# Optimization experiments

Measured on AMD Instinct MI355X. Metric: run time of the kernel, lower is better.

## Reference

```python
import jax, jax.numpy as jnp
import numpy as np
from math import sqrt

N = 8192      # points
I = 16        # in_channels
H = 64        # hidden_units
O = 64        # out_channels
CUTS = 8      # conv MLP intermediate width
RADIUS = 9.0
GROUPS = 4    # GroupNorm groups
BLK = 128     # i-block size for tiled pairwise reduction (KeOps-style)


def _leaky(x):
    return jnp.where(x >= 0, x, 0.2 * x)


def _group_norm(f, w, b, eps=1e-5):
    # torch GroupNorm applied to (1, C, N): stats per group over (C//G channels x N points)
    n, c = f.shape
    g = f.reshape(n, GROUPS, c // GROUPS)
    m = g.mean(axis=(0, 2), keepdims=True)
    v = ((g - m) ** 2).mean(axis=(0, 2), keepdims=True)
    g = (g - m) * jax.lax.rsqrt(v + eps)
    return g.reshape(n, c) * w + b


def setup_inputs() -> dict:
    key = jax.random.key(0)
    ks = jax.random.split(key, 20)
    U = lambda k, s, lim: jax.random.uniform(k, s, minval=-lim, maxval=lim)
    points = jax.random.normal(ks[0], (N, 3), dtype=jnp.float32)
    nuv = jax.random.normal(ks[1], (N, 3, 3), dtype=jnp.float32)
    features = jax.random.normal(ks[2], (N, I), dtype=jnp.float32)
    # net_in (torch Linear default init)
    W_in1 = U(ks[3], (H, I), 1 / np.sqrt(I)); b_in1 = U(ks[4], (H,), 1 / np.sqrt(I))
    W_in2 = U(ks[5], (H, H), 1 / np.sqrt(H)); b_in2 = U(ks[6], (H,), 1 / np.sqrt(H))
    # conv MLP with custom init from the module
    A1 = jax.random.normal(ks[7], (CUTS, 3), dtype=jnp.float32)
    B1 = jax.random.uniform(ks[8], (CUTS,)) * 0.8 * jnp.sqrt((A1 ** 2).sum(-1))
    A2 = U(ks[9], (H, CUTS), 1 / np.sqrt(CUTS))
    B2 = jax.random.normal(ks[10], (H,)) * 0.5 * jnp.sqrt((A2 ** 2).sum(-1))
    # net_out
    W_out1 = U(ks[11], (O, H), 1 / np.sqrt(H)); b_out1 = U(ks[12], (O,), 1 / np.sqrt(H))
    W_out2 = U(ks[13], (O, O), 1 / np.sqrt(O)); b_out2 = U(ks[14], (O,), 1 / np.sqrt(O))
    return {
        "points": points, "nuv": nuv, "features": features,
        "W_in1": W_in1, "b_in1": b_in1, "W_in2": W_in2, "b_in2": b_in2,
        "gn_in_w": jnp.ones((H,), jnp.float32), "gn_in_b": jnp.zeros((H,), jnp.float32),
        "A1": A1, "B1": B1, "A2": A2, "B2": B2,
        "W_out1": W_out1, "b_out1": b_out1, "W_out2": W_out2, "b_out2": b_out2,
        "gn_out_w": jnp.ones((O,), jnp.float32), "gn_out_b": jnp.zeros((O,), jnp.float32),
    }


def _forward(points, nuv, features, W_in1, b_in1, W_in2, b_in2, gn_in_w, gn_in_b,
             A1, B1, A2, B2, W_out1, b_out1, W_out2, b_out2, gn_out_w, gn_out_b):
    # 1. net_in + GroupNorm
    f = _leaky(features @ W_in1.T + b_in1)
    f = _leaky(f @ W_in2.T + b_in2)
    f = _group_norm(f, gn_in_w, gn_in_b)          # (N, H)
    # 2. quasi-geodesic interaction, tiled over i-blocks (KeOps-style)
    pts = points / (sqrt(2.0) * RADIUS)
    normals = jax.lax.stop_gradient(nuv[:, 0, :])  # n_j is detached in the original
    nblk = N // BLK

    def body(carry, blk):
        xi, nuvi = blk                              # (B,3), (B,3,3)
        ni = nuvi[:, 0, :]                          # (B,3) n_i (not detached)
        diff = pts[None, :, :] - xi[:, None, :]     # (B,N,3) x_j - x_i
        dn = ni @ normals.T                         # (B,N) <n_i, n_j>
        d2 = (diff ** 2).sum(-1) * (2.0 - dn) ** 2  # pseudo-geodesic squared dist
        w = jnp.exp(-d2)                            # Gaussian window
        X = jnp.einsum('bij,bnj->bni', nuvi, diff)  # coords in local basis (B,N,3)
        h = jax.nn.relu(jnp.einsum('bnj,cj->bnc', X, A1) + B1)   # (B,N,CUTS)
        g = jax.nn.relu(jnp.einsum('bnc,hc->bnh', h, A2) + B2)   # (B,N,H)
        out = jnp.einsum('bn,bnh,nh->bh', w, g, f)  # sum_j w_ij * conv(P_ij) * f_j
        return carry, out

    _, outs = jax.lax.scan(
        body, None, (pts.reshape(nblk, BLK, 3), nuv.reshape(nblk, BLK, 3, 3)))
    f2 = outs.reshape(N, H)
    # 3. net_out + GroupNorm
    f2 = _leaky(f2 @ W_out1.T + b_out1)
    f2 = _leaky(f2 @ W_out2.T + b_out2)
    f2 = _group_norm(f2, gn_out_w, gn_out_b)       # (N, O)
    return f2


def reference(points, nuv, features, W_in1, b_in1, W_in2, b_in2, gn_in_w, gn_in_b,
              A1, B1, A2, B2, W_out1, b_out1, W_out2, b_out2, gn_out_w, gn_out_b):
    return _forward(points, nuv, features, W_in1, b_in1, W_in2, b_in2, gn_in_w, gn_in_b,
                    A1, B1, A2, B2, W_out1, b_out1, W_out2, b_out2, gn_out_w, gn_out_b)
```

## Files before the change

### kernel.cpp

```cpp
#include <hip/hip_runtime.h>
#include <hip/hip_bf16.h>
#include <stdint.h>


#define N_PTS   8192
#define CHUNK   64
#define NCHUNK  (N_PTS / CHUNK)
#define WPB     8
#define PSCALE  0.07856742013183861f
#define GN_CNT  (N_PTS * 16)
#define FS_STRIDE 68

#define OFF_POINTS 0
#define OFF_NUV    24576
#define OFF_FEAT   98304
#define OFF_WIN1   229376
#define OFF_BIN1   230400
#define OFF_WIN2   230464
#define OFF_BIN2   234560
#define OFF_GNIW   234624
#define OFF_GNIB   234688
#define OFF_A1     234752
#define OFF_B1     234776
#define OFF_A2     234784
#define OFF_B2     235296
#define OFF_WOUT1  235360
#define OFF_BOUT1  239456
#define OFF_WOUT2  239520
#define OFF_BOUT2  243616
#define OFF_GNOW   243680
#define OFF_GNOB   243744
#define CVT_TOTAL  243808
#define NSEG 19

typedef _Float16 half2_t __attribute__((ext_vector_type(2)));
typedef _Float16 f16x8   __attribute__((ext_vector_type(8)));
typedef float    f32x4   __attribute__((ext_vector_type(4)));

struct InPtrs { const void* p[NSEG]; };

__device__ __forceinline__ float rfl(float x) {
  return __int_as_float(__builtin_amdgcn_readfirstlane(__float_as_int(x)));
}
__device__ __forceinline__ float leaky(float x) { return x > 0.f ? x : 0.2f * x; }

#if __has_builtin(__builtin_amdgcn_cvt_pkrtz)
__device__ __forceinline__ half2_t pk16(float a, float b) {
  return __builtin_bit_cast(half2_t, __builtin_amdgcn_cvt_pkrtz(a, b));
}
#else
__device__ __forceinline__ half2_t pk16(float a, float b) {
  half2_t r; r.x = (_Float16)a; r.y = (_Float16)b; return r;
}
#endif

__global__ __launch_bounds__(256) void prep_kernel(InPtrs ptrs, float* dst,
                                                   float* gstats) {
  if (blockIdx.x == 0 && threadIdx.x < 16) gstats[threadIdx.x] = 0.f;
  const uint32_t w0 = ((const uint32_t*)ptrs.p[7])[0];
  const bool bf = (w0 != 0x3F800000u);
  const int CUM[NSEG + 1] = {0, 24576, 98304, 229376, 230400, 230464, 234560,
                             234624, 234688, 234752, 234776, 234784, 235296,
                             235360, 239456, 239520, 243616, 243680, 243744,
                             243808};
  for (int e = blockIdx.x * 256 + threadIdx.x; e < CVT_TOTAL;
       e += gridDim.x * 256) {
    int s = 0;
#pragma unroll
    for (int i = 1; i < NSEG; ++i) s += (e >= CUM[i]) ? 1 : 0;
    const int rem = e - CUM[s];
    float v = bf ? __bfloat162float(((const __hip_bfloat16*)ptrs.p[s])[rem])
                 : ((const float*)ptrs.p[s])[rem];
    if (s == 0) v *= PSCALE;
    dst[e] = v;
  }
}

__global__ __launch_bounds__(256) void mlp_in_kernel(
    const float* __restrict__ pool, float* __restrict__ fbuf) {
  __shared__ float ls[4][64];
  const int t = threadIdx.x, nl = t >> 6, h = t & 63;
  const int n = blockIdx.x * 4 + nl;
  const float4* fr = (const float4*)(pool + OFF_FEAT + n * 16);
  const float4* w1 = (const float4*)(pool + OFF_WIN1 + h * 16);
  float a = pool[OFF_BIN1 + h];
#pragma unroll
  for (int k = 0; k < 4; ++k) {
    const float4 x = fr[k], w = w1[k];
    a = fmaf(x.x, w.x, a); a = fmaf(x.y, w.y, a);
    a = fmaf(x.z, w.z, a); a = fmaf(x.w, w.w, a);
  }
  ls[nl][h] = leaky(a);
  __syncthreads();
  const float4* w2 = (const float4*)(pool + OFF_WIN2 + h * 64);
  const float4* lr = (const float4*)&ls[nl][0];
  float c = pool[OFF_BIN2 + h];
#pragma unroll
  for (int k = 0; k < 16; ++k) {
    const float4 x = lr[k], w = w2[k];
    c = fmaf(x.x, w.x, c); c = fmaf(x.y, w.y, c);
    c = fmaf(x.z, w.z, c); c = fmaf(x.w, w.w, c);
  }
  fbuf[n * 64 + h] = leaky(c);
}

__global__ __launch_bounds__(256) void mlp_out_kernel(
    const float* __restrict__ cbuf, const float* __restrict__ pool,
    float* __restrict__ obuf) {
  __shared__ float ls[4][64];
  const int t = threadIdx.x, nl = t >> 6, h = t & 63;
  const int n = blockIdx.x * 4 + nl;
  const float4* cr = (const float4*)(cbuf + n * 64);
  const float4* w1 = (const float4*)(pool + OFF_WOUT1 + h * 64);
  float a = pool[OFF_BOUT1 + h];
#pragma unroll
  for (int k = 0; k < 16; ++k) {
    const float4 x = cr[k], w = w1[k];
    a = fmaf(x.x, w.x, a); a = fmaf(x.y, w.y, a);
    a = fmaf(x.z, w.z, a); a = fmaf(x.w, w.w, a);
  }
  ls[nl][h] = leaky(a);
  __syncthreads();
  const float4* w2 = (const float4*)(pool + OFF_WOUT2 + h * 64);
  const float4* lr = (const float4*)&ls[nl][0];
  float c = pool[OFF_BOUT2 + h];
#pragma unroll
  for (int k = 0; k < 16; ++k) {
    const float4 x = lr[k], w = w2[k];
    c = fmaf(x.x, w.x, c); c = fmaf(x.y, w.y, c);
    c = fmaf(x.z, w.z, c); c = fmaf(x.w, w.w, c);
  }
  obuf[n * 64 + h] = leaky(c);
}

__global__ __launch_bounds__(256) void gn_stats_kernel(
    const float* __restrict__ buf, float* __restrict__ gstats) {
  __shared__ float red[8];
  const int t = threadIdx.x;
  const int g = (t & 63) >> 4;
  if (t < 8) red[t] = 0.f;
  float s = 0.f, q = 0.f;
  for (int idx = blockIdx.x * 256 + t; idx < N_PTS * 64; idx += 64 * 256) {
    const float v = buf[idx];
    s += v; q = fmaf(v, v, q);
  }
  __syncthreads();
  atomicAdd(&red[g], s);
  atomicAdd(&red[4 + g], q);
  __syncthreads();
  if (t < 8) atomicAdd(&gstats[t], red[t]);
}

__global__ __launch_bounds__(256) void gn_apply_kernel(
    float* __restrict__ buf, const float* __restrict__ gstats,
    const float* __restrict__ pool) {
  const int idx = blockIdx.x * 256 + threadIdx.x;
  const int h = idx & 63, g = h >> 4;
  const float m = gstats[g] * (1.f / GN_CNT);
  const float v = gstats[4 + g] * (1.f / GN_CNT) - m * m;
  const float rs = rsqrtf(fmaxf(v, 0.f) + 1e-5f);
  buf[idx] = fmaf((buf[idx] - m) * rs, pool[OFF_GNIW + h], pool[OFF_GNIB + h]);
}

__global__ __launch_bounds__(256) void gn_apply_out_kernel(
    const float* __restrict__ buf, const float* __restrict__ gstats,
    const float* __restrict__ pool, void* __restrict__ out,
    const uint32_t* __restrict__ dref) {
  const bool bf = (dref[0] != 0x3F800000u);
  const int idx = blockIdx.x * 256 + threadIdx.x;
  const int h = idx & 63, g = h >> 4;
  const float m = gstats[g] * (1.f / GN_CNT);
  const float v = gstats[4 + g] * (1.f / GN_CNT) - m * m;
  const float rs = rsqrtf(fmaxf(v, 0.f) + 1e-5f);
  const float r = fmaf((buf[idx] - m) * rs, pool[OFF_GNOW + h], pool[OFF_GNOB + h]);
  if (bf) ((__hip_bfloat16*)out)[idx] = __float2bfloat16(r);
  else    ((float*)out)[idx] = r;
}

__global__ __launch_bounds__(512) void conv_kernel(
    const float* __restrict__ pool, const float* __restrict__ fbuf,
    float* __restrict__ cbuf) {
  __shared__ float  f_s[CHUNK * FS_STRIDE];
  __shared__ float4 hcA[WPB][4][32];
  __shared__ float4 zero4_s;

  const int t = threadIdx.x;
  const int wv = t >> 6, lane = t & 63;
  const int b = blockIdx.x * WPB + wv;
  const int kg  = lane >> 4;
  const int l15 = lane & 15;

  const float pbx = rfl(pool[OFF_POINTS + b * 3 + 0]);
  const float pby = rfl(pool[OFF_POINTS + b * 3 + 1]);
  const float pbz = rfl(pool[OFF_POINTS + b * 3 + 2]);
  float nb[9];
#pragma unroll
  for (int i = 0; i < 9; ++i) nb[i] = rfl(pool[OFF_NUV + b * 9 + i]);
  float a1v[24], b1v[8];
#pragma unroll
  for (int i = 0; i < 24; ++i) a1v[i] = rfl(pool[OFF_A1 + i]);
#pragma unroll
  for (int i = 0; i < 8; ++i)  b1v[i] = rfl(pool[OFF_B1 + i]);

  f16x8 bfrag[4];
#pragma unroll
  for (int ht = 0; ht < 4; ++ht) {
    const int h = 16 * ht + l15;
#pragma unroll
    for (int i = 0; i < 8; ++i) {
      float v = 0.f;
      if (kg == 0) v = pool[OFF_A2 + h * 8 + i];
      else if (kg == 1 && i == 0) v = pool[OFF_B2 + h];
      bfrag[ht][i] = (_Float16)v;
    }
  }

  {
    float4 z4; z4.x = 0.f; z4.y = 0.f; z4.z = 0.f; z4.w = 0.f;
    if (lane < 32) {
#pragma unroll
      for (int jt = 0; jt < 4; ++jt) hcA[wv][jt][lane] = z4;
    }
    if (t == 0) zero4_s = z4;
  }

  const f32x4 kzero = {0.f, 0.f, 0.f, 0.f};
  float acc[4] = {0.f, 0.f, 0.f, 0.f};
  const float4* fg4 = (const float4*)fbuf;

  for (int c = 0; c < NCHUNK; ++c) {
    const float4 fv0 = fg4[c * 1024 + t];
    const float4 fv1 = fg4[c * 1024 + t + 512];
    const int n = c * CHUNK + lane;
    const float px = pool[OFF_POINTS + n * 3 + 0];
    const float py = pool[OFF_POINTS + n * 3 + 1];
    const float pz = pool[OFF_POINTS + n * 3 + 2];
    const float nx = pool[OFF_NUV + n * 9 + 0];
    const float ny = pool[OFF_NUV + n * 9 + 1];
    const float nz = pool[OFF_NUV + n * 9 + 2];

    __syncthreads();
    ((float4*)f_s)[(t >> 4) * 17 + (t & 15)]        = fv0;
    ((float4*)f_s)[((t >> 4) + 32) * 17 + (t & 15)] = fv1;

    const float dx = px - pbx, dy = py - pby, dz = pz - pbz;
    const float X0 = fmaf(nb[0], dx, fmaf(nb[1], dy, nb[2] * dz));
    const float X1 = fmaf(nb[3], dx, fmaf(nb[4], dy, nb[5] * dz));
    const float X2 = fmaf(nb[6], dx, fmaf(nb[7], dy, nb[8] * dz));
    const float dn = fmaf(nb[0], nx, fmaf(nb[1], ny, nb[2] * nz));
    const float dd = fmaf(dx, dx, fmaf(dy, dy, dz * dz));
    const float tt = 2.f - dn;
    const float w = __expf(-dd * tt * tt);

    float hc[8];
#pragma unroll
    for (int cc = 0; cc < 8; ++cc)
      hc[cc] = w * fmaxf(fmaf(X0, a1v[cc * 3 + 0],
                         fmaf(X1, a1v[cc * 3 + 1],
                         fmaf(X2, a1v[cc * 3 + 2], b1v[cc]))), 0.f);
    float4 lo;
    lo.x = __builtin_bit_cast(float, pk16(hc[0], hc[1]));
    lo.y = __builtin_bit_cast(float, pk16(hc[2], hc[3]));
    lo.z = __builtin_bit_cast(float, pk16(hc[4], hc[5]));
    lo.w = __builtin_bit_cast(float, pk16(hc[6], hc[7]));
    hcA[wv][lane >> 4][l15] = lo;
    ((float*)&hcA[wv][lane >> 4][16 + l15])[0] =
        __builtin_bit_cast(float, pk16(w, 0.f));

    __syncthreads();

#pragma unroll
    for (int jt = 0; jt < 4; ++jt) {
      const float4* ap = (kg < 2) ? &hcA[wv][jt][kg * 16 + l15] : &zero4_s;
      const f16x8 af = __builtin_bit_cast(f16x8, *ap);
      const int fbase = (16 * jt + kg * 4) * FS_STRIDE + l15;
#pragma unroll
      for (int ht = 0; ht < 4; ++ht) {
        const f32x4 D = __builtin_amdgcn_mfma_f32_16x16x32_f16(
            af, bfrag[ht], kzero, 0, 0, 0);
        const float* fb = &f_s[fbase + 16 * ht];
#pragma unroll
        for (int r = 0; r < 4; ++r)
          acc[ht] = fmaf(fb[r * FS_STRIDE], fmaxf(D[r], 0.f), acc[ht]);
      }
    }
  }

#pragma unroll
  for (int ht = 0; ht < 4; ++ht) {
    acc[ht] += __shfl_xor(acc[ht], 16, 64);
    acc[ht] += __shfl_xor(acc[ht], 32, 64);
  }
  if (lane < 16) {
#pragma unroll
    for (int ht = 0; ht < 4; ++ht)
      cbuf[b * 64 + 16 * ht + lane] = acc[ht];
  }
}

extern "C" void kernel_launch(void* const* d_in, const int* in_sizes, int n_in,
                              void* d_out, int out_size, void* d_ws, size_t ws_size,
                              hipStream_t stream) {
  (void)in_sizes; (void)n_in; (void)out_size; (void)ws_size;
  const uint32_t* dref = (const uint32_t*)d_in[7];

  float* pool   = (float*)d_ws;
  float* fbuf   = pool + CVT_TOTAL;
  float* cbuf   = fbuf + N_PTS * 64;
  float* gstats = cbuf + N_PTS * 64;

  InPtrs ptrs;
  for (int i = 0; i < NSEG; ++i) ptrs.p[i] = d_in[i];

  prep_kernel<<<256, 256, 0, stream>>>(ptrs, pool, gstats);
  mlp_in_kernel<<<N_PTS / 4, 256, 0, stream>>>(pool, fbuf);
  gn_stats_kernel<<<64, 256, 0, stream>>>(fbuf, gstats);
  gn_apply_kernel<<<N_PTS * 64 / 256, 256, 0, stream>>>(fbuf, gstats, pool);
  conv_kernel<<<N_PTS / WPB, 512, 0, stream>>>(pool, fbuf, cbuf);
  mlp_out_kernel<<<N_PTS / 4, 256, 0, stream>>>(cbuf, pool, fbuf);
  gn_stats_kernel<<<64, 256, 0, stream>>>(fbuf, gstats + 8);
  gn_apply_out_kernel<<<N_PTS * 64 / 256, 256, 0, stream>>>(
      fbuf, gstats + 8, pool, d_out, dref);
}
```

Baseline: 699.2 us.

## Pre-pad normalized features and stream chunks into LDS via global_load_lds

The GroupNorm apply kernel now writes features into a chunked buffer that already has the padded LDS stride. The conv kernel can then copy each chunk straight from global memory into shared memory with global_load_lds DMA, instead of loading float4s into registers and storing them to LDS. The shared zero slot for inactive MFMA lanes becomes a zeroed padding entry inside hcA, which removes the per-lane pointer select. The aim is to cut VGPR use and VALU/LDS-store traffic in the hot loop. The trade-offs are an extra padded workspace buffer, and the loads are now issued after the barrier rather than prefetched ahead of it.

```diff
diff --git a/kernel.cpp b/kernel.cpp
--- a/kernel.cpp
+++ b/kernel.cpp
@@ -10,6 +10,7 @@
 #define PSCALE  0.07856742013183861f
 #define GN_CNT  (N_PTS * 16)
 #define FS_STRIDE 68
+#define CHUNK_FLOATS (CHUNK * FS_STRIDE)
 
 #define OFF_POINTS 0
 #define OFF_NUV    24576
@@ -36,6 +37,8 @@
 typedef _Float16 half2_t __attribute__((ext_vector_type(2)));
 typedef _Float16 f16x8   __attribute__((ext_vector_type(8)));
 typedef float    f32x4   __attribute__((ext_vector_type(4)));
+typedef __attribute__((address_space(3))) uint32_t lds_u32_t;
+typedef __attribute__((address_space(1))) const uint32_t glb_u32_t;
 
 struct InPtrs { const void* p[NSEG]; };
 
@@ -151,15 +154,16 @@
   if (t < 8) atomicAdd(&gstats[t], red[t]);
 }
 
-__global__ __launch_bounds__(256) void gn_apply_kernel(
-    float* __restrict__ buf, const float* __restrict__ gstats,
-    const float* __restrict__ pool) {
+__global__ __launch_bounds__(256) void gn_apply_pad_kernel(
+    const float* __restrict__ buf, const float* __restrict__ gstats,
+    const float* __restrict__ pool, float* __restrict__ fpad) {
   const int idx = blockIdx.x * 256 + threadIdx.x;
-  const int h = idx & 63, g = h >> 4;
+  const int h = idx & 63, n = idx >> 6, g = h >> 4;
   const float m = gstats[g] * (1.f / GN_CNT);
   const float v = gstats[4 + g] * (1.f / GN_CNT) - m * m;
   const float rs = rsqrtf(fmaxf(v, 0.f) + 1e-5f);
-  buf[idx] = fmaf((buf[idx] - m) * rs, pool[OFF_GNIW + h], pool[OFF_GNIB + h]);
+  const float r = fmaf((buf[idx] - m) * rs, pool[OFF_GNIW + h], pool[OFF_GNIB + h]);
+  fpad[(n >> 6) * CHUNK_FLOATS + (n & 63) * FS_STRIDE + h] = r;
 }
 
 __global__ __launch_bounds__(256) void gn_apply_out_kernel(
@@ -178,17 +182,17 @@
 }
 
 __global__ __launch_bounds__(512) void conv_kernel(
-    const float* __restrict__ pool, const float* __restrict__ fbuf,
+    const float* __restrict__ pool, const float* __restrict__ fpad,
     float* __restrict__ cbuf) {
-  __shared__ float  f_s[CHUNK * FS_STRIDE];
-  __shared__ float4 hcA[WPB][4][32];
-  __shared__ float4 zero4_s;
+  __shared__ float  f_s[CHUNK_FLOATS];
+  __shared__ float4 hcA[WPB][4][33];
 
   const int t = threadIdx.x;
   const int wv = t >> 6, lane = t & 63;
   const int b = blockIdx.x * WPB + wv;
   const int kg  = lane >> 4;
   const int l15 = lane & 15;
+  const int idx_fp = (kg < 2) ? (kg * 16 + l15) : 32;
 
   const float pbx = rfl(pool[OFF_POINTS + b * 3 + 0]);
   const float pby = rfl(pool[OFF_POINTS + b * 3 + 1]);
@@ -215,22 +219,16 @@
     }
   }
 
-  {
+  if (lane < 17) {
     float4 z4; z4.x = 0.f; z4.y = 0.f; z4.z = 0.f; z4.w = 0.f;
-    if (lane < 32) {
-#pragma unroll
-      for (int jt = 0; jt < 4; ++jt) hcA[wv][jt][lane] = z4;
-    }
-    if (t == 0) zero4_s = z4;
+#pragma unroll
+    for (int jt = 0; jt < 4; ++jt) hcA[wv][jt][16 + lane] = z4;
   }
 
   const f32x4 kzero = {0.f, 0.f, 0.f, 0.f};
   float acc[4] = {0.f, 0.f, 0.f, 0.f};
-  const float4* fg4 = (const float4*)fbuf;
 
   for (int c = 0; c < NCHUNK; ++c) {
-    const float4 fv0 = fg4[c * 1024 + t];
-    const float4 fv1 = fg4[c * 1024 + t + 512];
     const int n = c * CHUNK + lane;
     const float px = pool[OFF_POINTS + n * 3 + 0];
     const float py = pool[OFF_POINTS + n * 3 + 1];
@@ -240,8 +238,17 @@
     const float nz = pool[OFF_NUV + n * 9 + 2];
 
     __syncthreads();
-    ((float4*)f_s)[(t >> 4) * 17 + (t & 15)]        = fv0;
-    ((float4*)f_s)[((t >> 4) + 32) * 17 + (t & 15)] = fv1;
+
+    {
+      const glb_u32_t* src = (const glb_u32_t*)(fpad + c * CHUNK_FLOATS);
+      lds_u32_t* dst = (lds_u32_t*)f_s;
+      __builtin_amdgcn_global_load_lds(src + t * 4, dst + t * 4, 16, 0, 0);
+      __builtin_amdgcn_global_load_lds(src + 2048 + t * 4, dst + 2048 + t * 4,
+                                       16, 0, 0);
+      if (wv == 0)
+        __builtin_amdgcn_global_load_lds(src + 4096 + lane * 4,
+                                         dst + 4096 + lane * 4, 16, 0, 0);
+    }
 
     const float dx = px - pbx, dy = py - pby, dz = pz - pbz;
     const float X0 = fmaf(nb[0], dx, fmaf(nb[1], dy, nb[2] * dz));
@@ -271,8 +278,7 @@
 
 #pragma unroll
     for (int jt = 0; jt < 4; ++jt) {
-      const float4* ap = (kg < 2) ? &hcA[wv][jt][kg * 16 + l15] : &zero4_s;
-      const f16x8 af = __builtin_bit_cast(f16x8, *ap);
+      const f16x8 af = __builtin_bit_cast(f16x8, hcA[wv][jt][idx_fp]);
       const int fbase = (16 * jt + kg * 4) * FS_STRIDE + l15;
 #pragma unroll
       for (int ht = 0; ht < 4; ++ht) {
@@ -306,7 +312,8 @@
 
   float* pool   = (float*)d_ws;
   float* fbuf   = pool + CVT_TOTAL;
-  float* cbuf   = fbuf + N_PTS * 64;
+  float* fpad   = fbuf + N_PTS * 64;
+  float* cbuf   = fpad + NCHUNK * CHUNK_FLOATS;
   float* gstats = cbuf + N_PTS * 64;
 
   InPtrs ptrs;
@@ -315,8 +322,9 @@
   prep_kernel<<<256, 256, 0, stream>>>(ptrs, pool, gstats);
   mlp_in_kernel<<<N_PTS / 4, 256, 0, stream>>>(pool, fbuf);
   gn_stats_kernel<<<64, 256, 0, stream>>>(fbuf, gstats);
-  gn_apply_kernel<<<N_PTS * 64 / 256, 256, 0, stream>>>(fbuf, gstats, pool);
-  conv_kernel<<<N_PTS / WPB, 512, 0, stream>>>(pool, fbuf, cbuf);
+  gn_apply_pad_kernel<<<N_PTS * 64 / 256, 256, 0, stream>>>(fbuf, gstats, pool,
+                                                            fpad);
+  conv_kernel<<<N_PTS / WPB, 512, 0, stream>>>(pool, fpad, cbuf);
   mlp_out_kernel<<<N_PTS / 4, 256, 0, stream>>>(cbuf, pool, fbuf);
   gn_stats_kernel<<<64, 256, 0, stream>>>(fbuf, gstats + 8);
   gn_apply_out_kernel<<<N_PTS * 64 / 256, 256, 0, stream>>>(
```

New measurement: 726.3 us. 3.9% more time.
